# Optimization experiments

Hardware: AMD Instinct MI355X
Metric: run time of the kernel (lower is better)

Reference implementation:

```python
import jax, jax.numpy as jnp
import numpy as np

D_MODEL = 1024
NUM_HEADS = 16


def _linear(x, W, b):
    # torch nn.Linear: y = x @ W.T + b
    return jnp.einsum('bsd,od->bso', x, W) + b


def _split_heads(x, H):
    B, S, D = x.shape
    return x.reshape(B, S, H, D // H).transpose(0, 2, 1, 3)  # [B,H,S,dk]


def setup_inputs() -> dict:
    key0 = jax.random.key(0)
    ks = jax.random.split(key0, 11)
    B, S, D = 4, 2048, D_MODEL
    w_scale = 1.0 / np.sqrt(D)
    inp = {
        'query': jax.random.normal(ks[0], (B, S, D), jnp.float32),
        'key': jax.random.normal(ks[1], (B, S, D), jnp.float32),
        'value': jax.random.normal(ks[2], (B, S, D), jnp.float32),
        'Wq': jax.random.normal(ks[3], (D, D), jnp.float32) * w_scale,
        'bq': jax.random.normal(ks[4], (D,), jnp.float32) * 0.01,
        'Wk': jax.random.normal(ks[5], (D, D), jnp.float32) * w_scale,
        'bk': jax.random.normal(ks[6], (D,), jnp.float32) * 0.01,
        'Wv': jax.random.normal(ks[7], (D, D), jnp.float32) * w_scale,
        'bv': jax.random.normal(ks[8], (D,), jnp.float32) * 0.01,
        'Wo': jax.random.normal(ks[9], (D, D), jnp.float32) * w_scale,
        'bo': jax.random.normal(ks[10], (D,), jnp.float32) * 0.01,
        'common_prefix_len': 1792,
    }
    return inp


def reference(query, key, value, Wq, bq, Wk, bk, Wv, bv, Wo, bo, common_prefix_len):
    B, S, D = query.shape
    H = NUM_HEADS
    dk = D // H
    P = common_prefix_len
    scale = 1.0 / np.sqrt(dk)

    Q = _split_heads(_linear(query, Wq, bq), H)  # [B,H,S,dk]
    K = _split_heads(_linear(key, Wk, bk), H)
    V = _split_heads(_linear(value, Wv, bv), H)

    # --- prefix: causal self-attention over first P tokens ---
    Qp, Kp, Vp = Q[:, :, :P], K[:, :, :P], V[:, :, :P]
    sp = jnp.einsum('bhld,bhsd->bhls', Qp, Kp) * scale  # [B,H,P,P]
    causal = jnp.tril(jnp.ones((P, P), dtype=bool))
    sp = jnp.where(causal, sp, -jnp.inf)
    prefix_ctx = jnp.einsum('bhls,bhsd->bhld', jax.nn.softmax(sp, axis=-1), Vp)

    # --- candidates: attend to full prefix + own diagonal entry ---
    Qc = Q[:, :, P:]  # [B,H,N,dk]
    N = S - P
    sc = jnp.einsum('bhld,bhsd->bhls', Qc, K) * scale  # [B,H,N,S]
    mask = jnp.concatenate(
        [jnp.ones((N, P), dtype=bool), jnp.eye(N, dtype=bool)], axis=-1)  # [N,S]
    sc = jnp.where(mask, sc, -jnp.inf)
    cand_ctx = jnp.einsum('bhls,bhsd->bhld', jax.nn.softmax(sc, axis=-1), V)

    ctx = jnp.concatenate([prefix_ctx, cand_ctx], axis=2)  # [B,H,S,dk]
    ctx = ctx.transpose(0, 2, 1, 3).reshape(B, S, D)
    return _linear(ctx, Wo, bo)
```

## Files before the change

kernel.cpp:

```cpp
#include <hip/hip_runtime.h>
#include <hip/hip_bf16.h>
#include <stdint.h>
#include <stddef.h>

#define D_M   1024
#define N_H   16
#define D_K   64
#define S_LEN 2048
#define N_B   4
#define P_LEN 1792
#define M_ROWS (N_B*S_LEN)

#define QSCALE 0.1803368801111601f

typedef unsigned short u16;
typedef __bf16  bf16x8 __attribute__((ext_vector_type(8)));
typedef __bf16  bf16x4 __attribute__((ext_vector_type(4)));
typedef __bf16  bf16x2 __attribute__((ext_vector_type(2)));
typedef float   f32x4  __attribute__((ext_vector_type(4)));
typedef float   f32x16 __attribute__((ext_vector_type(16)));
typedef unsigned u32x2 __attribute__((ext_vector_type(2)));
typedef unsigned u32x4 __attribute__((ext_vector_type(4)));

#define MFMA32(a,b,c)   __builtin_amdgcn_mfma_f32_16x16x32_bf16((a),(b),(c),0,0,0)
#define MFMA3216(a,b,c) __builtin_amdgcn_mfma_f32_32x32x16_bf16((a),(b),(c),0,0,0)

__device__ __forceinline__ float ex2(float x){
#if defined(__HIP_DEVICE_COMPILE__) && __has_builtin(__builtin_amdgcn_exp2f)
  return __builtin_amdgcn_exp2f(x);
#else
  return exp2f(x);
#endif
}

#define GLDS16(gp, lp) __builtin_amdgcn_global_load_lds( \
    (__attribute__((address_space(1))) void*)(gp), \
    (__attribute__((address_space(3))) void*)(lp), 16, 0, 0)

__device__ __forceinline__ u16 f2bf(float f){
  unsigned u = __builtin_bit_cast(unsigned, f);
  u += 0x7FFFu + ((u>>16)&1u);
  return (u16)(u>>16);
}

__device__ __forceinline__ unsigned pkbf(float a, float b){
  bf16x2 t; t[0] = (__bf16)a; t[1] = (__bf16)b;
  return __builtin_bit_cast(unsigned, t);
}

__device__ __forceinline__ void plswap(unsigned &x, unsigned &y){
  asm("v_permlane32_swap_b32 %0, %1" : "+v"(x), "+v"(y));
}

__global__ void cvt_bf16(const float* __restrict__ in, u16* __restrict__ out, int n8){
  typedef u16 u16x8 __attribute__((ext_vector_type(8)));
  for (int i = blockIdx.x*blockDim.x + threadIdx.x; i < n8; i += gridDim.x*blockDim.x){
    const float4* p = (const float4*)(in + (size_t)i*8);
    float4 a = p[0], b = p[1];
    u16x8 o;
    o[0]=f2bf(a.x); o[1]=f2bf(a.y); o[2]=f2bf(a.z); o[3]=f2bf(a.w);
    o[4]=f2bf(b.x); o[5]=f2bf(b.y); o[6]=f2bf(b.z); o[7]=f2bf(b.w);
    *(u16x8*)(out + (size_t)i*8) = o;
  }
}

template<int MODE, int SWZ, int CVT>
__global__ __launch_bounds__(256, CVT ? 2 : 3)
void gemm_bt(const void* __restrict__ Ain, const u16* __restrict__ Bm,
             const float* __restrict__ bias, void* __restrict__ Cout, float scale)
{
  constexpr int Kd = 1024, N = 1024, NT = Kd/32;
  __shared__ __align__(16) u16 As[128*32];
  __shared__ __align__(16) u16 Bs[128*32];
  const int tid  = threadIdx.x;
  const int wid  = tid >> 6, lane = tid & 63;
  const int rowBase = blockIdx.x * 128, colBase = blockIdx.y * 128;

  const int srow = (wid<<4) + (lane>>2);
  const int scol = (lane&3) << 3;
  const u16*  A16 = (const u16*)Ain;
  const float* A32 = (const float*)Ain;

  const u16* Ag0 = A16 + (size_t)(rowBase + srow)*Kd + scol;
  const u16* Ag1 = Ag0 + (size_t)64*Kd;
  const float* Af = A32 + (size_t)(rowBase + (tid>>3))*Kd + ((tid&7)<<2);
  u16* AsD = As + (tid>>3)*32 + ((tid&7)<<2);
  float4 a4[4];

  const u16* Bg0 = Bm + (size_t)(colBase + srow)*Kd + scol;
  const u16* Bg1 = Bg0 + (size_t)64*Kd;
  u16* AsW0 = As + (wid<<9);
  u16* AsW1 = As + 2048 + (wid<<9);
  u16* BsW0 = Bs + (wid<<9);
  u16* BsW1 = Bs + 2048 + (wid<<9);

  f32x4 acc[4][4] = {};
  const int fr = lane & 15, fk = (lane>>4) << 3;
  const int wr = (wid>>1) << 6, wc = (wid&1) << 6;

#define ISSUEA(KO) do{ _Pragma("unroll") \
    for (int g=0; g<4; ++g) a4[g] = *(const float4*)(Af + (KO) + (size_t)(g*32)*Kd); }while(0)

  if (CVT) ISSUEA(0);

  for (int kt = 0; kt < NT; ++kt){
    const int ko = kt*32;
    __syncthreads();
    if (CVT){
#pragma unroll
      for (int g=0; g<4; ++g){
        u32x2 w2 = { pkbf(a4[g].x, a4[g].y), pkbf(a4[g].z, a4[g].w) };
        *(u32x2*)(AsD + g*1024) = w2;
      }
      GLDS16(Bg0+ko, BsW0); GLDS16(Bg1+ko, BsW1);
      if (kt+1 < NT) ISSUEA(ko + 32);
    } else {
      GLDS16(Ag0+ko, AsW0); GLDS16(Ag1+ko, AsW1);
      GLDS16(Bg0+ko, BsW0); GLDS16(Bg1+ko, BsW1);
    }
    __syncthreads();
    bf16x8 af[4], bf[4];
#pragma unroll
    for (int i=0;i<4;++i) af[i] = *(const bf16x8*)&As[(wr + i*16 + fr)*32 + fk];
#pragma unroll
    for (int i=0;i<4;++i) bf[i] = *(const bf16x8*)&Bs[(wc + i*16 + fr)*32 + fk];
#pragma unroll
    for (int i=0;i<4;++i)
#pragma unroll
      for (int j=0;j<4;++j)
        acc[i][j] = MFMA32(af[i], bf[j], acc[i][j]);
  }
#undef ISSUEA

  const int rr0 = (lane>>4) << 2;
#pragma unroll
  for (int i=0;i<4;++i){
#pragma unroll
    for (int j=0;j<4;++j){
      const int gc = colBase + wc + j*16 + fr;
      const float bb = bias[gc];
#pragma unroll
      for (int r=0;r<4;++r){
        const int gr = rowBase + wr + i*16 + rr0 + r;
        const float v = (acc[i][j][r] + bb) * scale;
        if (MODE == 2){
          ((float*)Cout)[(size_t)gr*N + gc] = v;
        } else {
          const int b = gr >> 11, s = gr & 2047;
          const int hh = gc >> 6, k = gc & 63;
          if (MODE == 0){
            const int kk = SWZ ? ((k&7) | ((((k>>3) ^ (s&7)))<<3)) : k;
            ((u16*)Cout)[(((size_t)(b*N_H + hh))*S_LEN + s)*D_K + kk] = f2bf(v);
          } else {
            const int ss = SWZ ? ((s & ~63) | (s&7) | (((((s>>3)&7) ^ (k&7)))<<3)) : s;
            ((u16*)Cout)[(((size_t)(b*N_H + hh))*D_K + k)*S_LEN + ss] = f2bf(v);
          }
        }
      }
    }
  }
}


__device__ __forceinline__ void attn_self(
    const u16* __restrict__ Kb, const u16* __restrict__ Vb,
    const bf16x8* qf, int ks0, int h, int q,
    float& l, f32x16& o0, f32x16& o1)
{
  bf16x8 kr[4];
  {
    const int rr = ks0 + q, sw = rr & 7;
    const u16* kp = Kb + (size_t)rr * D_K;
#pragma unroll
    for (int kb=0;kb<4;++kb)
      kr[kb] = *(const bf16x8*)(kp + (((h + 2*kb) ^ sw) << 3));
  }
  f32x16 s0 = {};
  __builtin_amdgcn_s_setprio(1);
#pragma unroll
  for (int kb=0;kb<4;++kb) s0 = MFMA3216(kr[kb], qf[kb], s0);
  __builtin_amdgcn_s_setprio(0);

  bf16x8 v0[4];
  {
    const int gb = ks0 & ~63, lc0 = (ks0 - gb) >> 3;
    const int sw = q & 7;
#pragma unroll
    for (int db=0;db<2;++db){
      const u16* vp = Vb + (size_t)(32*db + q)*S_LEN + gb;
      v0[2*db]   = *(const bf16x8*)(vp + (((lc0 + h    ) ^ sw) << 3));
      v0[2*db+1] = *(const bf16x8*)(vp + (((lc0 + h + 2) ^ sw) << 3));
    }
  }

  float a[16];
#pragma unroll
  for (int r=0;r<16;++r){
    const int krow = (r&3) + 8*(r>>2) + 4*h;
    float p0 = (krow == q) ? ex2(s0[r]) : 0.f;
    s0[r] = p0; a[r] = p0;
  }
#pragma unroll
  for (int w=8; w>=1; w>>=1)
#pragma unroll
    for (int r=0;r<w;++r) a[r] += a[r+w];
  l += a[0] + __shfl_xor(a[0], 32, 64);

  unsigned w0[8];
#pragma unroll
  for (int i=0;i<8;++i) w0[i] = pkbf(s0[2*i], s0[2*i+1]);
  plswap(w0[0],w0[2]); plswap(w0[1],w0[3]);
  plswap(w0[4],w0[6]); plswap(w0[5],w0[7]);
  bf16x8 p00 = __builtin_bit_cast(bf16x8, (u32x4){w0[0],w0[1],w0[2],w0[3]});
  bf16x8 p01 = __builtin_bit_cast(bf16x8, (u32x4){w0[4],w0[5],w0[6],w0[7]});

  __builtin_amdgcn_s_setprio(1);
  o0 = MFMA3216(v0[0], p00, o0);
  o1 = MFMA3216(v0[2], p00, o1);
  o0 = MFMA3216(v0[1], p01, o0);
  o1 = MFMA3216(v0[3], p01, o1);
  __builtin_amdgcn_s_setprio(0);
}

template<int MASKED>
__device__ __forceinline__ void steplds(
    const u16* __restrict__ Ksb, const u16* __restrict__ Vsb,
    const bf16x8* qf, int ks, int qg, int h, int q,
    float& l, f32x16& o0, f32x16& o1)
{
  bf16x8 kr[8];
#pragma unroll
  for (int s=0;s<2;++s){
    const int rr = 32*s + q, base = rr*64, sw = rr&7;
#pragma unroll
    for (int kb=0;kb<4;++kb)
      kr[4*s+kb] = *(const bf16x8*)&Ksb[base + (((h + 2*kb)^sw)<<3)];
  }
  f32x16 s0 = {}, s1 = {};
  __builtin_amdgcn_s_setprio(1);
#pragma unroll
  for (int kb=0;kb<4;++kb){
    s0 = MFMA3216(kr[kb],   qf[kb], s0);
    s1 = MFMA3216(kr[4+kb], qf[kb], s1);
  }
  __builtin_amdgcn_s_setprio(0);

  bf16x8 v0[4], v1[4];
#pragma unroll
  for (int db=0;db<2;++db){
    const int rd = 32*db + q, base = rd*64, sw = rd&7;
    v0[2*db]   = *(const bf16x8*)&Vsb[base + (((h    )^sw)<<3)];
    v0[2*db+1] = *(const bf16x8*)&Vsb[base + (((h + 2)^sw)<<3)];
    v1[2*db]   = *(const bf16x8*)&Vsb[base + (((h + 4)^sw)<<3)];
    v1[2*db+1] = *(const bf16x8*)&Vsb[base + (((h + 6)^sw)<<3)];
  }

  if (MASKED){
#pragma unroll
    for (int r=0;r<16;++r){
      const int krow = (r&3) + 8*(r>>2) + 4*h;
      if (ks + krow      > qg) s0[r] = -1e30f;
      if (ks + 32 + krow > qg) s1[r] = -1e30f;
    }
  }

  float a[16];
#pragma unroll
  for (int r=0;r<16;++r){
    float p0 = ex2(s0[r]); s0[r] = p0;
    float p1 = ex2(s1[r]); s1[r] = p1;
    a[r] = p0 + p1;
  }
#pragma unroll
  for (int w=8; w>=1; w>>=1)
#pragma unroll
    for (int r=0;r<w;++r) a[r] += a[r+w];
  l += a[0] + __shfl_xor(a[0], 32, 64);

  unsigned w0[8];
#pragma unroll
  for (int i=0;i<8;++i) w0[i] = pkbf(s0[2*i], s0[2*i+1]);
  plswap(w0[0],w0[2]); plswap(w0[1],w0[3]);
  plswap(w0[4],w0[6]); plswap(w0[5],w0[7]);
  bf16x8 p00 = __builtin_bit_cast(bf16x8, (u32x4){w0[0],w0[1],w0[2],w0[3]});
  bf16x8 p01 = __builtin_bit_cast(bf16x8, (u32x4){w0[4],w0[5],w0[6],w0[7]});
  unsigned w1[8];
#pragma unroll
  for (int i=0;i<8;++i) w1[i] = pkbf(s1[2*i], s1[2*i+1]);
  plswap(w1[0],w1[2]); plswap(w1[1],w1[3]);
  plswap(w1[4],w1[6]); plswap(w1[5],w1[7]);
  bf16x8 p10 = __builtin_bit_cast(bf16x8, (u32x4){w1[0],w1[1],w1[2],w1[3]});
  bf16x8 p11 = __builtin_bit_cast(bf16x8, (u32x4){w1[4],w1[5],w1[6],w1[7]});

  __builtin_amdgcn_s_setprio(1);
  o0 = MFMA3216(v0[0], p00, o0);
  o1 = MFMA3216(v0[2], p00, o1);
  o0 = MFMA3216(v0[1], p01, o0);
  o1 = MFMA3216(v0[3], p01, o1);
  o0 = MFMA3216(v1[0], p10, o0);
  o1 = MFMA3216(v1[2], p10, o1);
  o0 = MFMA3216(v1[1], p11, o0);
  o1 = MFMA3216(v1[3], p11, o1);
  __builtin_amdgcn_s_setprio(0);
}

__device__ __forceinline__ void attn_write(
    u16* __restrict__ ctx, int bh, int qg, int h,
    float inv, const f32x16& o0, const f32x16& o1)
{
  const int b = bh >> 4, hd = bh & 15;
  u16* cp = ctx + ((size_t)b*S_LEN + qg)*D_M + hd*D_K;
#pragma unroll
  for (int rg=0; rg<4; ++rg){
    const int d0 = 8*rg + 4*h;
    bf16x4 oa, ob;
#pragma unroll
    for (int e=0;e<4;++e){ oa[e] = (__bf16)(o0[4*rg+e]*inv); ob[e] = (__bf16)(o1[4*rg+e]*inv); }
    *(bf16x4*)(cp + d0)      = oa;
    *(bf16x4*)(cp + 32 + d0) = ob;
  }
}

__global__ __launch_bounds__(128)
void attn_all(const u16* __restrict__ Q, const u16* __restrict__ K,
              const u16* __restrict__ Vt, u16* __restrict__ ctx)
{
  __shared__ __align__(16) u16 Ksm[2][4096];
  __shared__ __align__(16) u16 Vsm[2][4096];

  const int x = blockIdx.x;
  const int type = x >> 6, bh = x & 63;
  const int wid = threadIdx.x >> 6, lane = threadIdx.x & 63;
  const int q = lane & 31, h = lane >> 5;
  const bool iscand = (type < 4);
  const int tt = 31 - type;
  const int qb = iscand ? (P_LEN + (type<<6) + (wid<<5)) : ((tt<<6) + (wid<<5));
  const int nsteps = iscand ? (P_LEN/64) : (tt+1);
  const int qg = qb + q;

  const u16* Kb = K  + (size_t)bh * S_LEN * D_K;
  const u16* Vb = Vt + (size_t)bh * D_K * S_LEN;
  const u16* Qp = Q + ((size_t)bh * S_LEN + qg) * D_K + (h<<3);
  bf16x8 qf[4];
#pragma unroll
  for (int kb=0;kb<4;++kb) qf[kb] = *(const bf16x8*)(Qp + 16*kb);

  float l = 0.f;
  f32x16 o0 = {}, o1 = {};

  const int rl = lane >> 3, cl = (lane & 7) << 3;
  const int rb = wid << 5;

#define STAGE(T, B) do{                                                        \
    const int _ks = (T) << 6;                                                  \
    _Pragma("unroll")                                                          \
    for (int g=0; g<4; ++g){                                                   \
      const int _r = rb + (g<<3);                                              \
      GLDS16(Kb + (size_t)(_ks + _r + rl)*D_K + cl,   &Ksm[B][_r<<6]);         \
      GLDS16(Vb + (size_t)(_r + rl)*S_LEN + _ks + cl, &Vsm[B][_r<<6]);         \
    }                                                                          \
  }while(0)

  STAGE(0, 0);
  __syncthreads();

  for (int t = 0; t < nsteps; ++t){
    if (t+1 < nsteps) STAGE(t+1, (t+1)&1);
    if (!iscand && t == nsteps-1)
      steplds<1>(Ksm[t&1], Vsm[t&1], qf, t<<6, qg, h, q, l, o0, o1);
    else
      steplds<0>(Ksm[t&1], Vsm[t&1], qf, t<<6, qg, h, q, l, o0, o1);
    __syncthreads();
  }
#undef STAGE

  if (iscand)
    attn_self(Kb, Vb, qf, qb, h, q, l, o0, o1);

  attn_write(ctx, bh, qg, h, 1.f/l, o0, o1);
}

extern "C" void kernel_launch(void* const* d_in, const int* in_sizes, int n_in,
                              void* d_out, int out_size, void* d_ws, size_t ws_size,
                              hipStream_t stream)
{
  const float* query = (const float*)d_in[0];
  const float* key   = (const float*)d_in[1];
  const float* value = (const float*)d_in[2];
  const float* Wq = (const float*)d_in[3];
  const float* bq = (const float*)d_in[4];
  const float* Wk = (const float*)d_in[5];
  const float* bk = (const float*)d_in[6];
  const float* Wv = (const float*)d_in[7];
  const float* bv = (const float*)d_in[8];
  const float* Wo = (const float*)d_in[9];
  const float* bo = (const float*)d_in[10];

  if (ws_size < (size_t)(66u<<20)) return;

  char* ws = (char*)d_ws;
  u16* ctx = (u16*)(ws);
  u16* Wb  = (u16*)(ws + (16u<<20));
  u16* Qb  = (u16*)(ws + (18u<<20));
  u16* Kb  = (u16*)(ws + (34u<<20));
  u16* Vb  = (u16*)(ws + (50u<<20));

  const int nW8 = (D_M*D_M)/8;
  dim3 gg(M_ROWS/128, D_M/128);

  cvt_bf16<<<512,256,0,stream>>>(Wq, Wb, nW8);
  gemm_bt<0,0,1><<<gg,256,0,stream>>>(query, Wb, bq, Qb, QSCALE);

  cvt_bf16<<<512,256,0,stream>>>(Wk, Wb, nW8);
  gemm_bt<0,1,1><<<gg,256,0,stream>>>(key, Wb, bk, Kb, 1.0f);

  cvt_bf16<<<512,256,0,stream>>>(Wv, Wb, nW8);
  gemm_bt<1,1,1><<<gg,256,0,stream>>>(value, Wb, bv, Vb, 1.0f);

  attn_all<<<dim3(2048), 128, 0, stream>>>(Qb, Kb, Vb, ctx);

  cvt_bf16<<<512,256,0,stream>>>(Wo, Wb, nW8);
  gemm_bt<2,0,0><<<gg,256,0,stream>>>(ctx, Wb, bo, (float*)d_out, 1.0f);
}
```

Before: 199.3 us.

## Stage fp32 A tiles directly to LDS with swizzle, convert to bf16 at fragment load

In the CVT variant of the projection GEMM, the fp32 activations are now copied straight into shared memory with global-to-LDS loads, using an XOR swizzle on the column index. Previously they were staged through registers, converted, and stored to LDS. The bf16 packing now happens when each MFMA fragment is read from LDS. This drops the register prefetch, so the launch bound can rise to 3 blocks per CU, at the cost of doubling A's LDS footprint and doing conversion work per fragment read.

```diff
diff --git a/kernel.cpp b/kernel.cpp
--- a/kernel.cpp
+++ b/kernel.cpp
@@ -65,12 +65,12 @@
 }
 
 template<int MODE, int SWZ, int CVT>
-__global__ __launch_bounds__(256, CVT ? 2 : 3)
+__global__ __launch_bounds__(256,3)
 void gemm_bt(const void* __restrict__ Ain, const u16* __restrict__ Bm,
              const float* __restrict__ bias, void* __restrict__ Cout, float scale)
 {
   constexpr int Kd = 1024, N = 1024, NT = Kd/32;
-  __shared__ __align__(16) u16 As[128*32];
+  __shared__ __align__(16) u16 As[(CVT ? 64 : 32)*128];
   __shared__ __align__(16) u16 Bs[128*32];
   const int tid  = threadIdx.x;
   const int wid  = tid >> 6, lane = tid & 63;
@@ -83,9 +83,9 @@
 
   const u16* Ag0 = A16 + (size_t)(rowBase + srow)*Kd + scol;
   const u16* Ag1 = Ag0 + (size_t)64*Kd;
-  const float* Af = A32 + (size_t)(rowBase + (tid>>3))*Kd + ((tid&7)<<2);
-  u16* AsD = As + (tid>>3)*32 + ((tid&7)<<2);
-  float4 a4[4];
+  const float* Asrc0 = A32 + (size_t)(rowBase + (tid>>3))*Kd
+                           + (((tid&7) ^ ((tid>>3)&7)) << 2);
+  float* AsF = (float*)As;
 
   const u16* Bg0 = Bm + (size_t)(colBase + srow)*Kd + scol;
   const u16* Bg1 = Bg0 + (size_t)64*Kd;
@@ -98,30 +98,35 @@
   const int fr = lane & 15, fk = (lane>>4) << 3;
   const int wr = (wid>>1) << 6, wc = (wid&1) << 6;
 
-#define ISSUEA(KO) do{ _Pragma("unroll") \
-    for (int g=0; g<4; ++g) a4[g] = *(const float4*)(Af + (KO) + (size_t)(g*32)*Kd); }while(0)
-
-  if (CVT) ISSUEA(0);
-
   for (int kt = 0; kt < NT; ++kt){
     const int ko = kt*32;
     __syncthreads();
     if (CVT){
 #pragma unroll
-      for (int g=0; g<4; ++g){
-        u32x2 w2 = { pkbf(a4[g].x, a4[g].y), pkbf(a4[g].z, a4[g].w) };
-        *(u32x2*)(AsD + g*1024) = w2;
-      }
-      GLDS16(Bg0+ko, BsW0); GLDS16(Bg1+ko, BsW1);
-      if (kt+1 < NT) ISSUEA(ko + 32);
+      for (int g=0; g<4; ++g)
+        GLDS16(Asrc0 + ko + (size_t)(32*g)*Kd, AsF + (32*g + wid*8)*32);
     } else {
       GLDS16(Ag0+ko, AsW0); GLDS16(Ag1+ko, AsW1);
-      GLDS16(Bg0+ko, BsW0); GLDS16(Bg1+ko, BsW1);
     }
+    GLDS16(Bg0+ko, BsW0); GLDS16(Bg1+ko, BsW1);
     __syncthreads();
     bf16x8 af[4], bf[4];
-#pragma unroll
-    for (int i=0;i<4;++i) af[i] = *(const bf16x8*)&As[(wr + i*16 + fr)*32 + fk];
+    if (CVT){
+      const int hh2 = (fk>>3) << 1;
+#pragma unroll
+      for (int i=0;i<4;++i){
+        const int rr = wr + i*16 + fr, s = rr & 7;
+        const float4* rp = (const float4*)(AsF + rr*32);
+        float4 lo = rp[hh2 ^ s];
+        float4 hi = rp[(hh2|1) ^ s];
+        af[i] = __builtin_bit_cast(bf16x8,
+            (u32x4){ pkbf(lo.x,lo.y), pkbf(lo.z,lo.w),
+                     pkbf(hi.x,hi.y), pkbf(hi.z,hi.w) });
+      }
+    } else {
+#pragma unroll
+      for (int i=0;i<4;++i) af[i] = *(const bf16x8*)&As[(wr + i*16 + fr)*32 + fk];
+    }
 #pragma unroll
     for (int i=0;i<4;++i) bf[i] = *(const bf16x8*)&Bs[(wc + i*16 + fr)*32 + fk];
 #pragma unroll
@@ -130,7 +135,6 @@
       for (int j=0;j<4;++j)
         acc[i][j] = MFMA32(af[i], bf[j], acc[i][j]);
   }
-#undef ISSUEA
 
   const int rr0 = (lane>>4) << 2;
 #pragma unroll
```

New measurement: 200.1 us. About the same (+0.4%).
